# Optimization experiments

Hardware: AMD Instinct MI355X
Metric: run time of the kernel (lower is better)

Reference implementation:

```python
import jax, jax.numpy as jnp
import numpy as np

B, S, D = 2, 2048, 1024
H = 16
HD = D // H  # 64
SCALE = HD ** 0.5


def setup_inputs() -> dict:
    key = jax.random.key(0)
    ks = jax.random.split(key, 7)
    return {
        "query": jax.random.normal(ks[0], (B, S, D), dtype=jnp.float32),
        "key": jax.random.normal(ks[1], (B, S, D), dtype=jnp.float32),
        "value": jax.random.normal(ks[2], (B, S, D), dtype=jnp.float32),
        "W_qkv_w": jax.random.normal(ks[3], (3 * D, 3 * D), dtype=jnp.float32) * (1.0 / np.sqrt(3 * D)),
        "W_qkv_b": jax.random.normal(ks[4], (3 * D,), dtype=jnp.float32) * 0.02,
        "W_o_w": jax.random.normal(ks[5], (D, D), dtype=jnp.float32) * (1.0 / np.sqrt(D)),
        "W_o_b": jax.random.normal(ks[6], (D,), dtype=jnp.float32) * 0.02,
    }


def _split_heads(x):
    # [B,S,D] -> [B,H,S,HD]
    return x.reshape(B, S, H, HD).transpose(0, 2, 1, 3)


def reference(query, key, value, W_qkv_w, W_qkv_b, W_o_w, W_o_b):
    # fused QKV projection: concat then Linear(3D, 3D)  (torch: x @ W.T + b)
    qkv = jnp.concatenate([query, key, value], axis=-1)
    qkv = qkv @ W_qkv_w.T + W_qkv_b
    q, k, v = jnp.split(qkv, 3, axis=-1)
    q, k, v = _split_heads(q), _split_heads(k), _split_heads(v)
    # naive attention: materializes [B,H,S,S]
    scores = jnp.einsum('bhqd,bhkd->bhqk', q, k) / SCALE
    probs = jax.nn.softmax(scores, axis=-1)
    attn = jnp.einsum('bhqk,bhkd->bhqd', probs, v)
    # combine heads: [B,H,S,HD] -> [B,S,D]
    attn = attn.transpose(0, 2, 1, 3).reshape(B, S, D)
    return attn @ W_o_w.T + W_o_b
```

## Files before the change

### kernel.cpp

```cpp
#include <hip/hip_runtime.h>
#include <cmath>

#define BS   2
#define SEQ  2048
#define DM   1024
#define NH   16
#define HD   64
#define D3   3072
#define MROWS 4096
#define KVBLK 64
#define QBLK  128
#define NTILES (SEQ / KVBLK)

typedef _Float16 f16;
typedef __attribute__((ext_vector_type(4))) _Float16 half4;
typedef __attribute__((ext_vector_type(8))) _Float16 half8;
typedef __attribute__((ext_vector_type(4))) float f32x4;
typedef unsigned int u32;
typedef __attribute__((ext_vector_type(4))) u32 u32x4;

__device__ __forceinline__ void async_cp16(const void* g, void* s) {
    __builtin_amdgcn_global_load_lds(
        (const __attribute__((address_space(1))) u32*)g,
        (__attribute__((address_space(3))) u32*)s, 16, 0, 0);
}

__global__ __launch_bounds__(256) void conv_concat_kernel(
    const float* __restrict__ q, const float* __restrict__ k,
    const float* __restrict__ v, f16* __restrict__ out)
{
    const int seg = blockIdx.x;
    const int row = blockIdx.y;
    const int c   = threadIdx.x * 4;
    const float* src = (seg == 0 ? q : (seg == 1 ? k : v)) + (size_t)row * DM + c;
    float4 x = *(const float4*)src;
    half4 h = {(f16)x.x, (f16)x.y, (f16)x.z, (f16)x.w};
    *(half4*)&out[(size_t)row * D3 + seg * DM + c] = h;
}

__global__ __launch_bounds__(256) void conv_plain_kernel(
    const float* __restrict__ src, f16* __restrict__ dst, int n4)
{
    int i = blockIdx.x * 256 + threadIdx.x;
    const int stride = gridDim.x * 256;
    for (; i < n4; i += stride) {
        float4 x = *(const float4*)&src[(size_t)i * 4];
        half4 h = {(f16)x.x, (f16)x.y, (f16)x.z, (f16)x.w};
        *(half4*)&dst[(size_t)i * 4] = h;
    }
}

template<int KDIM, int NDIM, bool F16OUT>
__global__ __launch_bounds__(256) void gemm_f16_kernel(
    const f16* __restrict__ A, const f16* __restrict__ W,
    const float* __restrict__ bias, void* __restrict__ Cout)
{
    __shared__ f16 As[128 * 32];
    __shared__ f16 Ws[128 * 32];

    const int tid  = threadIdx.x;
    const int lane = tid & 63;
    const int wave = tid >> 6;
    const int l15  = lane & 15;
    const int lg   = lane >> 4;
    const int wm   = wave >> 1;
    const int wn   = wave & 1;

    const int cpx = gridDim.x >> 3;
    const int lid = (blockIdx.x & 7) * cpx + (blockIdx.x >> 3);
    const int NT  = NDIM / 128;
    const int tM0 = (lid / NT) * 128;
    const int tN0 = (lid % NT) * 128;

    const int srow = lane >> 2;
    const int sch  = lane & 3;
    const int ssc  = sch ^ ((srow >> 1) & 3);

    const f16* gA0 = A + (size_t)(tM0 + wave * 32      + srow) * KDIM + ssc * 8;
    const f16* gA1 = A + (size_t)(tM0 + wave * 32 + 16 + srow) * KDIM + ssc * 8;
    const f16* gW0 = W + (size_t)(tN0 + wave * 32      + srow) * KDIM + ssc * 8;
    const f16* gW1 = W + (size_t)(tN0 + wave * 32 + 16 + srow) * KDIM + ssc * 8;
    f16* lA0 = &As[(wave * 32)      * 32];
    f16* lA1 = &As[(wave * 32 + 16) * 32];
    f16* lW0 = &Ws[(wave * 32)      * 32];
    f16* lW1 = &Ws[(wave * 32 + 16) * 32];

    f32x4 acc[4][4];
#pragma unroll
    for (int i = 0; i < 4; ++i)
#pragma unroll
        for (int j = 0; j < 4; ++j) acc[i][j] = (f32x4){0.f, 0.f, 0.f, 0.f};

    const int fsw = (lg ^ ((l15 >> 1) & 3)) * 8;
    int aoff[4], woff[4];
#pragma unroll
    for (int mi = 0; mi < 4; ++mi) aoff[mi] = (wm * 64 + mi * 16 + l15) * 32 + fsw;
#pragma unroll
    for (int ni = 0; ni < 4; ++ni) woff[ni] = (wn * 64 + ni * 16 + l15) * 32 + fsw;

    for (int k0 = 0; k0 < KDIM; k0 += 32) {
        __syncthreads();
        async_cp16(gA0 + k0, lA0);
        async_cp16(gA1 + k0, lA1);
        async_cp16(gW0 + k0, lW0);
        async_cp16(gW1 + k0, lW1);
        __syncthreads();

        half8 af[4], wf[4];
#pragma unroll
        for (int mi = 0; mi < 4; ++mi) af[mi] = *(half8*)&As[aoff[mi]];
#pragma unroll
        for (int ni = 0; ni < 4; ++ni) wf[ni] = *(half8*)&Ws[woff[ni]];
#pragma unroll
        for (int mi = 0; mi < 4; ++mi)
#pragma unroll
            for (int ni = 0; ni < 4; ++ni)
                acc[mi][ni] = __builtin_amdgcn_mfma_f32_16x16x32_f16(
                    af[mi], wf[ni], acc[mi][ni], 0, 0, 0);
    }

    float bv[4];
#pragma unroll
    for (int ni = 0; ni < 4; ++ni) bv[ni] = bias[tN0 + wn * 64 + ni * 16 + l15];

#pragma unroll
    for (int mi = 0; mi < 4; ++mi)
#pragma unroll
        for (int ni = 0; ni < 4; ++ni)
#pragma unroll
            for (int r = 0; r < 4; ++r) {
                const int m   = tM0 + wm * 64 + mi * 16 + lg * 4 + r;
                const int col = tN0 + wn * 64 + ni * 16 + l15;
                const float val = acc[mi][ni][r] + bv[ni];
                if constexpr (F16OUT)
                    ((f16*)Cout)[(size_t)m * NDIM + col] = (f16)val;
                else
                    ((float*)Cout)[(size_t)m * NDIM + col] = val;
            }
}


#define V_STORE(VtN, va, vb) do {                                             \
    u32x4 aw_ = __builtin_bit_cast(u32x4, va);                                \
    u32x4 bw_ = __builtin_bit_cast(u32x4, vb);                                \
    _Pragma("unroll")                                                         \
    for (int wd_ = 0; wd_ < 4; ++wd_) {                                       \
        u32 lo_ = __builtin_amdgcn_perm(bw_[wd_], aw_[wd_], 0x05040100u);     \
        u32 hi_ = __builtin_amdgcn_perm(bw_[wd_], aw_[wd_], 0x07060302u);     \
        const int dl_ = vd0 + 2 * wd_;                                        \
        const int dh_ = dl_ + 1;                                              \
        *(u32*)&VtN[dl_ * KVBLK + (((vp >> 2) ^ (dl_ & 7) ^ (dl_ >> 3)) * 8)  \
                    + 2 * (vp & 3)] = lo_;                                    \
        *(u32*)&VtN[dh_ * KVBLK + (((vp >> 2) ^ (dh_ & 7) ^ (dh_ >> 3)) * 8)  \
                    + 2 * (vp & 3)] = hi_;                                    \
    }                                                                         \
} while (0)

#define ATTN_STEP(KhC, VtC, KhN, VtN, TT, PF) do {                            \
    half8 va_ = {}, vb_ = {};                                                 \
    if (PF) {                                                                 \
        const size_t nro_ = (size_t)((TT) + 1) * KVBLK;                       \
        async_cp16(kxsrc + (nro_ + wave * 16 +     krow_l) * D3,              \
                   &KhN[(wave * 16) * HD]);                                   \
        async_cp16(kxsrc + (nro_ + wave * 16 + 8 + krow_l) * D3,              \
                   &KhN[(wave * 16 + 8) * HD]);                               \
        va_ = *(const half8*)(vsrc0 + nro_ * D3);                             \
        vb_ = *(const half8*)(vsrc0 + nro_ * D3 + D3);                        \
    }                                                                         \
    f32x4 sc[2][4];                                                           \
    _Pragma("unroll")                                                         \
    for (int rt = 0; rt < 2; ++rt)                                            \
        _Pragma("unroll")                                                     \
        for (int ct = 0; ct < 4; ++ct) sc[rt][ct] = (f32x4){0.f,0.f,0.f,0.f}; \
    __builtin_amdgcn_s_setprio(1);                                            \
    _Pragma("unroll")                                                         \
    for (int ct = 0; ct < 4; ++ct) {                                          \
        const int krow = ct * 16 + l15;                                       \
        _Pragma("unroll")                                                     \
        for (int ks = 0; ks < 2; ++ks) {                                      \
            half8 kf = *(half8*)&KhC[krow * HD +                              \
                                     (((ks * 4 + lg) ^ (krow & 7)) * 8)];     \
            _Pragma("unroll")                                                 \
            for (int rt = 0; rt < 2; ++rt)                                    \
                sc[rt][ct] = __builtin_amdgcn_mfma_f32_16x16x32_f16(          \
                    qf[rt][ks], kf, sc[rt][ct], 0, 0, 0);                     \
        }                                                                     \
    }                                                                         \
    __builtin_amdgcn_s_setprio(0);                                            \
    _Pragma("unroll")                                                         \
    for (int rt = 0; rt < 2; ++rt)                                            \
        _Pragma("unroll")                                                     \
        for (int ct = 0; ct < 4; ++ct)                                        \
            _Pragma("unroll")                                                 \
            for (int r = 0; r < 4; ++r) sc[rt][ct][r] *= 0.125f;              \
    _Pragma("unroll")                                                         \
    for (int rt = 0; rt < 2; ++rt) {                                          \
        float mt[4];                                                          \
        _Pragma("unroll")                                                     \
        for (int r = 0; r < 4; ++r)                                           \
            mt[r] = fmaxf(fmaxf(sc[rt][0][r], sc[rt][1][r]),                  \
                          fmaxf(sc[rt][2][r], sc[rt][3][r]));                 \
        _Pragma("unroll")                                                     \
        for (int m = 1; m < 16; m <<= 1)                                      \
            _Pragma("unroll")                                                 \
            for (int r = 0; r < 4; ++r)                                       \
                mt[r] = fmaxf(mt[r], __shfl_xor(mt[r], m));                   \
        float alpha[4], mn[4];                                                \
        _Pragma("unroll")                                                     \
        for (int r = 0; r < 4; ++r) {                                         \
            mn[r] = fmaxf(mrun[rt][r], mt[r]);                                \
            alpha[r] = __expf(mrun[rt][r] - mn[r]);                           \
            mrun[rt][r] = mn[r];                                              \
        }                                                                     \
        float ls[4] = {0.f, 0.f, 0.f, 0.f};                                   \
        _Pragma("unroll")                                                     \
        for (int ct = 0; ct < 4; ++ct) {                                      \
            f32x4 v = sc[rt][ct];                                             \
            _Pragma("unroll")                                                 \
            for (int r = 0; r < 4; ++r) {                                     \
                v[r] = __expf(v[r] - mn[r]);                                  \
                ls[r] += v[r];                                                \
                const int qq = rt * 16 + lg * 4 + r;                          \
                const int chP = (ct * 2 + (l15 >> 3)) ^ (lg << 1);            \
                Pl[pbase + qq * KVBLK + chP * 8 + (l15 & 7)] = (f16)v[r];     \
            }                                                                 \
        }                                                                     \
        _Pragma("unroll")                                                     \
        for (int m = 1; m < 16; m <<= 1)                                      \
            _Pragma("unroll")                                                 \
            for (int r = 0; r < 4; ++r) ls[r] += __shfl_xor(ls[r], m);        \
        _Pragma("unroll")                                                     \
        for (int r = 0; r < 4; ++r)                                           \
            lrun[rt][r] = lrun[rt][r] * alpha[r] + ls[r];                     \
        _Pragma("unroll")                                                     \
        for (int dct = 0; dct < 4; ++dct)                                     \
            _Pragma("unroll")                                                 \
            for (int r = 0; r < 4; ++r) oacc[rt][dct][r] *= alpha[r];         \
    }                                                                         \
    __builtin_amdgcn_s_setprio(1);                                            \
    _Pragma("unroll")                                                         \
    for (int ks2 = 0; ks2 < 2; ++ks2) {                                       \
        half8 pa[2];                                                          \
        _Pragma("unroll")                                                     \
        for (int rt = 0; rt < 2; ++rt) {                                      \
            const int qq = rt * 16 + l15;                                     \
            const int chR = (ks2 * 4 + lg) ^ ((l15 >> 2) << 1);               \
            pa[rt] = *(half8*)&Pl[pbase + qq * KVBLK + chR * 8];              \
        }                                                                     \
        _Pragma("unroll")                                                     \
        for (int dct = 0; dct < 4; ++dct) {                                   \
            const int d = dct * 16 + l15;                                     \
            half8 vf = *(half8*)&VtC[d * KVBLK +                              \
                        (((ks2 * 4 + lg) ^ (d & 7) ^ (d >> 3)) * 8)];         \
            _Pragma("unroll")                                                 \
            for (int rt = 0; rt < 2; ++rt)                                    \
                oacc[rt][dct] = __builtin_amdgcn_mfma_f32_16x16x32_f16(       \
                    pa[rt], vf, oacc[rt][dct], 0, 0, 0);                      \
        }                                                                     \
    }                                                                         \
    __builtin_amdgcn_s_setprio(0);                                            \
    if (PF) { V_STORE(VtN, va_, vb_); }                                       \
    __syncthreads();                                                          \
} while (0)

__global__ __launch_bounds__(256, 2) void attn_mfma_kernel(
    const f16* __restrict__ qkvh, f16* __restrict__ attnh)
{
    __shared__ f16 Kh0[KVBLK * HD];
    __shared__ f16 Kh1[KVBLK * HD];
    __shared__ f16 Vt0[HD * KVBLK];
    __shared__ f16 Vt1[HD * KVBLK];
    __shared__ f16 Pl[4 * 32 * KVBLK];

    const int tid  = threadIdx.x;
    const int lane = tid & 63;
    const int wave = tid >> 6;
    const int l15  = lane & 15;
    const int lg   = lane >> 4;

    const int nq  = SEQ / QBLK;
    const int bid = blockIdx.x;
    const int b   = bid / (NH * nq);
    const int h   = (bid / nq) % NH;
    const int qc  = bid % nq;
    const int q0  = qc * QBLK + wave * 32;
    const size_t bS = (size_t)b * SEQ;

    const int krow_l = lane >> 3;
    const int kschk  = (lane & 7) ^ krow_l;
    const f16* kxsrc = qkvh + bS * D3 + DM + h * HD + kschk * 8;

    const int vp  = tid >> 3;
    const int vd0 = (tid & 7) * 8;
    const f16* vsrc0 = qkvh + (bS + 2 * vp) * D3 + 2 * DM + h * HD + vd0;

    half8 qf[2][2];
#pragma unroll
    for (int rt = 0; rt < 2; ++rt)
#pragma unroll
        for (int ks = 0; ks < 2; ++ks)
            qf[rt][ks] = *(const half8*)&qkvh[(bS + q0 + rt * 16 + l15) * D3 +
                                              h * HD + ks * 32 + lg * 8];

    f32x4 oacc[2][4];
#pragma unroll
    for (int rt = 0; rt < 2; ++rt)
#pragma unroll
        for (int dct = 0; dct < 4; ++dct) oacc[rt][dct] = (f32x4){0.f, 0.f, 0.f, 0.f};

    float mrun[2][4], lrun[2][4];
#pragma unroll
    for (int rt = 0; rt < 2; ++rt)
#pragma unroll
        for (int r = 0; r < 4; ++r) { mrun[rt][r] = -INFINITY; lrun[rt][r] = 0.f; }

    const int pbase = wave * 32 * KVBLK;

    {
        async_cp16(kxsrc + (size_t)(wave * 16 +     krow_l) * D3, &Kh0[(wave * 16) * HD]);
        async_cp16(kxsrc + (size_t)(wave * 16 + 8 + krow_l) * D3, &Kh0[(wave * 16 + 8) * HD]);
        half8 va_ = *(const half8*)(vsrc0);
        half8 vb_ = *(const half8*)(vsrc0 + D3);
        V_STORE(Vt0, va_, vb_);
        __syncthreads();
    }

    for (int t = 0; t < NTILES; t += 2) {
        ATTN_STEP(Kh0, Vt0, Kh1, Vt1, t, true);
        ATTN_STEP(Kh1, Vt1, Kh0, Vt0, t + 1, (t + 1) < (NTILES - 1));
    }

#pragma unroll
    for (int rt = 0; rt < 2; ++rt) {
        float inv[4];
#pragma unroll
        for (int r = 0; r < 4; ++r) inv[r] = 1.f / lrun[rt][r];
#pragma unroll
        for (int dct = 0; dct < 4; ++dct)
#pragma unroll
            for (int r = 0; r < 4; ++r) {
                const int qq = q0 + rt * 16 + lg * 4 + r;
                attnh[(bS + qq) * DM + h * HD + dct * 16 + l15] =
                    (f16)(oacc[rt][dct][r] * inv[r]);
            }
    }
}

extern "C" void kernel_launch(void* const* d_in, const int* in_sizes, int n_in,
                              void* d_out, int out_size, void* d_ws, size_t ws_size,
                              hipStream_t stream) {
    const float* q    = (const float*)d_in[0];
    const float* k    = (const float*)d_in[1];
    const float* v    = (const float*)d_in[2];
    const float* Wqkv = (const float*)d_in[3];
    const float* bqkv = (const float*)d_in[4];
    const float* Wo   = (const float*)d_in[5];
    const float* bo   = (const float*)d_in[6];
    float* out = (float*)d_out;

    char* ws = (char*)d_ws;
    f16* Ain    = (f16*)ws;
    f16* attn_h = (f16*)ws;
    f16* Wo_h   = (f16*)(ws + 16777216);
    f16* Wqkv_h = (f16*)(ws + 25165824);
    f16* qkv_h  = (f16*)(ws + 44040192);

    conv_concat_kernel<<<dim3(3, MROWS), 256, 0, stream>>>(q, k, v, Ain);
    conv_plain_kernel<<<2048, 256, 0, stream>>>(Wqkv, Wqkv_h, D3 * D3 / 4);

    gemm_f16_kernel<D3, D3, true><<<dim3((MROWS / 128) * (D3 / 128)), 256, 0, stream>>>(
        Ain, Wqkv_h, bqkv, qkv_h);

    attn_mfma_kernel<<<dim3(BS * NH * (SEQ / QBLK)), 256, 0, stream>>>(qkv_h, attn_h);

    conv_plain_kernel<<<512, 256, 0, stream>>>(Wo, Wo_h, DM * DM / 4);

    gemm_f16_kernel<DM, DM, false><<<dim3((MROWS / 128) * (DM / 128)), 256, 0, stream>>>(
        attn_h, Wo_h, bo, out);
}
```

Measured before the change: 242.9 us.

## Shrink attention query block to 64 rows with one 16-row tile per wave

Halves the query block so each wave handles a single 16-row tile instead of two. This cuts accumulator registers and P-tile shared memory, and raises launch bounds to 4 blocks per CU to improve occupancy and latency hiding. It also remaps block IDs across 8 groups (XCD-aware swizzle) so that blocks sharing K/V land together. In exchange, each K/V tile loaded into LDS is reused by half as many query rows, doubling K/V traffic and the per-tile load and sync overhead relative to the MFMA work.

```diff
diff --git a/kernel.cpp b/kernel.cpp
--- a/kernel.cpp
+++ b/kernel.cpp
@@ -9,7 +9,7 @@
 #define D3   3072
 #define MROWS 4096
 #define KVBLK 64
-#define QBLK  128
+#define QBLK  64
 #define NTILES (SEQ / KVBLK)
 
 typedef _Float16 f16;
@@ -167,11 +167,9 @@
         va_ = *(const half8*)(vsrc0 + nro_ * D3);                             \
         vb_ = *(const half8*)(vsrc0 + nro_ * D3 + D3);                        \
     }                                                                         \
-    f32x4 sc[2][4];                                                           \
-    _Pragma("unroll")                                                         \
-    for (int rt = 0; rt < 2; ++rt)                                            \
-        _Pragma("unroll")                                                     \
-        for (int ct = 0; ct < 4; ++ct) sc[rt][ct] = (f32x4){0.f,0.f,0.f,0.f}; \
+    f32x4 sc[4];                                                              \
+    _Pragma("unroll")                                                         \
+    for (int ct = 0; ct < 4; ++ct) sc[ct] = (f32x4){0.f, 0.f, 0.f, 0.f};      \
     __builtin_amdgcn_s_setprio(1);                                            \
     _Pragma("unroll")                                                         \
     for (int ct = 0; ct < 4; ++ct) {                                          \
@@ -180,26 +178,21 @@
         for (int ks = 0; ks < 2; ++ks) {                                      \
             half8 kf = *(half8*)&KhC[krow * HD +                              \
                                      (((ks * 4 + lg) ^ (krow & 7)) * 8)];     \
-            _Pragma("unroll")                                                 \
-            for (int rt = 0; rt < 2; ++rt)                                    \
-                sc[rt][ct] = __builtin_amdgcn_mfma_f32_16x16x32_f16(          \
-                    qf[rt][ks], kf, sc[rt][ct], 0, 0, 0);                     \
+            sc[ct] = __builtin_amdgcn_mfma_f32_16x16x32_f16(                  \
+                qf[ks], kf, sc[ct], 0, 0, 0);                                 \
         }                                                                     \
     }                                                                         \
     __builtin_amdgcn_s_setprio(0);                                            \
     _Pragma("unroll")                                                         \
-    for (int rt = 0; rt < 2; ++rt)                                            \
-        _Pragma("unroll")                                                     \
-        for (int ct = 0; ct < 4; ++ct)                                        \
-            _Pragma("unroll")                                                 \
-            for (int r = 0; r < 4; ++r) sc[rt][ct][r] *= 0.125f;              \
-    _Pragma("unroll")                                                         \
-    for (int rt = 0; rt < 2; ++rt) {                                          \
+    for (int ct = 0; ct < 4; ++ct)                                            \
+        _Pragma("unroll")                                                     \
+        for (int r = 0; r < 4; ++r) sc[ct][r] *= 0.125f;                      \
+    {                                                                         \
         float mt[4];                                                          \
         _Pragma("unroll")                                                     \
         for (int r = 0; r < 4; ++r)                                           \
-            mt[r] = fmaxf(fmaxf(sc[rt][0][r], sc[rt][1][r]),                  \
-                          fmaxf(sc[rt][2][r], sc[rt][3][r]));                 \
+            mt[r] = fmaxf(fmaxf(sc[0][r], sc[1][r]),                          \
+                          fmaxf(sc[2][r], sc[3][r]));                         \
         _Pragma("unroll")                                                     \
         for (int m = 1; m < 16; m <<= 1)                                      \
             _Pragma("unroll")                                                 \
@@ -208,19 +201,19 @@
         float alpha[4], mn[4];                                                \
         _Pragma("unroll")                                                     \
         for (int r = 0; r < 4; ++r) {                                         \
-            mn[r] = fmaxf(mrun[rt][r], mt[r]);                                \
-            alpha[r] = __expf(mrun[rt][r] - mn[r]);                           \
-            mrun[rt][r] = mn[r];                                              \
+            mn[r] = fmaxf(mrun[r], mt[r]);                                    \
+            alpha[r] = __expf(mrun[r] - mn[r]);                               \
+            mrun[r] = mn[r];                                                  \
         }                                                                     \
         float ls[4] = {0.f, 0.f, 0.f, 0.f};                                   \
         _Pragma("unroll")                                                     \
         for (int ct = 0; ct < 4; ++ct) {                                      \
-            f32x4 v = sc[rt][ct];                                             \
+            f32x4 v = sc[ct];                                                 \
             _Pragma("unroll")                                                 \
             for (int r = 0; r < 4; ++r) {                                     \
                 v[r] = __expf(v[r] - mn[r]);                                  \
                 ls[r] += v[r];                                                \
-                const int qq = rt * 16 + lg * 4 + r;                          \
+                const int qq = lg * 4 + r;                                    \
                 const int chP = (ct * 2 + (l15 >> 3)) ^ (lg << 1);            \
                 Pl[pbase + qq * KVBLK + chP * 8 + (l15 & 7)] = (f16)v[r];     \
             }                                                                 \
@@ -230,32 +223,25 @@
             _Pragma("unroll")                                                 \
             for (int r = 0; r < 4; ++r) ls[r] += __shfl_xor(ls[r], m);        \
         _Pragma("unroll")                                                     \
-        for (int r = 0; r < 4; ++r)                                           \
-            lrun[rt][r] = lrun[rt][r] * alpha[r] + ls[r];                     \
+        for (int r = 0; r < 4; ++r) lrun[r] = lrun[r] * alpha[r] + ls[r];     \
         _Pragma("unroll")                                                     \
         for (int dct = 0; dct < 4; ++dct)                                     \
             _Pragma("unroll")                                                 \
-            for (int r = 0; r < 4; ++r) oacc[rt][dct][r] *= alpha[r];         \
+            for (int r = 0; r < 4; ++r) oacc[dct][r] *= alpha[r];             \
     }                                                                         \
     __builtin_amdgcn_s_setprio(1);                                            \
     _Pragma("unroll")                                                         \
     for (int ks2 = 0; ks2 < 2; ++ks2) {                                       \
-        half8 pa[2];                                                          \
-        _Pragma("unroll")                                                     \
-        for (int rt = 0; rt < 2; ++rt) {                                      \
-            const int qq = rt * 16 + l15;                                     \
-            const int chR = (ks2 * 4 + lg) ^ ((l15 >> 2) << 1);               \
-            pa[rt] = *(half8*)&Pl[pbase + qq * KVBLK + chR * 8];              \
-        }                                                                     \
+        const int qq = l15;                                                   \
+        const int chR = (ks2 * 4 + lg) ^ ((l15 >> 2) << 1);                   \
+        half8 pa = *(half8*)&Pl[pbase + qq * KVBLK + chR * 8];                \
         _Pragma("unroll")                                                     \
         for (int dct = 0; dct < 4; ++dct) {                                   \
             const int d = dct * 16 + l15;                                     \
             half8 vf = *(half8*)&VtC[d * KVBLK +                              \
                         (((ks2 * 4 + lg) ^ (d & 7) ^ (d >> 3)) * 8)];         \
-            _Pragma("unroll")                                                 \
-            for (int rt = 0; rt < 2; ++rt)                                    \
-                oacc[rt][dct] = __builtin_amdgcn_mfma_f32_16x16x32_f16(       \
-                    pa[rt], vf, oacc[rt][dct], 0, 0, 0);                      \
+            oacc[dct] = __builtin_amdgcn_mfma_f32_16x16x32_f16(               \
+                pa, vf, oacc[dct], 0, 0, 0);                                  \
         }                                                                     \
     }                                                                         \
     __builtin_amdgcn_s_setprio(0);                                            \
@@ -263,14 +249,14 @@
     __syncthreads();                                                          \
 } while (0)
 
-__global__ __launch_bounds__(256, 2) void attn_mfma_kernel(
+__global__ __launch_bounds__(256, 4) void attn_mfma_kernel(
     const f16* __restrict__ qkvh, f16* __restrict__ attnh)
 {
     __shared__ f16 Kh0[KVBLK * HD];
     __shared__ f16 Kh1[KVBLK * HD];
     __shared__ f16 Vt0[HD * KVBLK];
     __shared__ f16 Vt1[HD * KVBLK];
-    __shared__ f16 Pl[4 * 32 * KVBLK];
+    __shared__ f16 Pl[4 * 16 * KVBLK];
 
     const int tid  = threadIdx.x;
     const int lane = tid & 63;
@@ -279,11 +265,12 @@
     const int lg   = lane >> 4;
 
     const int nq  = SEQ / QBLK;
-    const int bid = blockIdx.x;
-    const int b   = bid / (NH * nq);
-    const int h   = (bid / nq) % NH;
-    const int qc  = bid % nq;
-    const int q0  = qc * QBLK + wave * 32;
+    const int cpx = gridDim.x >> 3;
+    const int lid = (blockIdx.x & 7) * cpx + (blockIdx.x >> 3);
+    const int b   = lid / (NH * nq);
+    const int h   = (lid / nq) % NH;
+    const int qc  = lid % nq;
+    const int q0  = qc * QBLK + wave * 16;
     const size_t bS = (size_t)b * SEQ;
 
     const int krow_l = lane >> 3;
@@ -294,27 +281,21 @@
     const int vd0 = (tid & 7) * 8;
     const f16* vsrc0 = qkvh + (bS + 2 * vp) * D3 + 2 * DM + h * HD + vd0;
 
-    half8 qf[2][2];
-#pragma unroll
-    for (int rt = 0; rt < 2; ++rt)
-#pragma unroll
-        for (int ks = 0; ks < 2; ++ks)
-            qf[rt][ks] = *(const half8*)&qkvh[(bS + q0 + rt * 16 + l15) * D3 +
-                                              h * HD + ks * 32 + lg * 8];
-
-    f32x4 oacc[2][4];
-#pragma unroll
-    for (int rt = 0; rt < 2; ++rt)
-#pragma unroll
-        for (int dct = 0; dct < 4; ++dct) oacc[rt][dct] = (f32x4){0.f, 0.f, 0.f, 0.f};
-
-    float mrun[2][4], lrun[2][4];
-#pragma unroll
-    for (int rt = 0; rt < 2; ++rt)
-#pragma unroll
-        for (int r = 0; r < 4; ++r) { mrun[rt][r] = -INFINITY; lrun[rt][r] = 0.f; }
-
-    const int pbase = wave * 32 * KVBLK;
+    half8 qf[2];
+#pragma unroll
+    for (int ks = 0; ks < 2; ++ks)
+        qf[ks] = *(const half8*)&qkvh[(bS + q0 + l15) * D3 +
+                                      h * HD + ks * 32 + lg * 8];
+
+    f32x4 oacc[4];
+#pragma unroll
+    for (int dct = 0; dct < 4; ++dct) oacc[dct] = (f32x4){0.f, 0.f, 0.f, 0.f};
+
+    float mrun[4], lrun[4];
+#pragma unroll
+    for (int r = 0; r < 4; ++r) { mrun[r] = -INFINITY; lrun[r] = 0.f; }
+
+    const int pbase = wave * 16 * KVBLK;
 
     {
         async_cp16(kxsrc + (size_t)(wave * 16 +     krow_l) * D3, &Kh0[(wave * 16) * HD]);
@@ -330,18 +311,17 @@
         ATTN_STEP(Kh1, Vt1, Kh0, Vt0, t + 1, (t + 1) < (NTILES - 1));
     }
 
-#pragma unroll
-    for (int rt = 0; rt < 2; ++rt) {
+    {
         float inv[4];
 #pragma unroll
-        for (int r = 0; r < 4; ++r) inv[r] = 1.f / lrun[rt][r];
+        for (int r = 0; r < 4; ++r) inv[r] = 1.f / lrun[r];
 #pragma unroll
         for (int dct = 0; dct < 4; ++dct)
 #pragma unroll
             for (int r = 0; r < 4; ++r) {
-                const int qq = q0 + rt * 16 + lg * 4 + r;
+                const int qq = q0 + lg * 4 + r;
                 attnh[(bS + qq) * DM + h * HD + dct * 16 + l15] =
-                    (f16)(oacc[rt][dct][r] * inv[r]);
+                    (f16)(oacc[dct][r] * inv[r]);
             }
     }
 }
```

After: 253.4 us. 1.04x slower.

## Transpose attention MFMA operands so softmax rows live per lane, use exp2

Applied to the files above, without the earlier changes.

Swaps the MFMA A/B operands for both QK^T and PV so each lane owns a single query row. Row max and sum then need only two cross-lane shuffles instead of four per register. The scale is folded into an exp2 argument via FMA. P is packed with cvt_pkrtz and written with 8-byte LDS stores under a new XOR swizzle, and the output is stored as half4 vectors. Block IDs are also remapped across 8 groups, likely to spread work over XCDs for cache locality. The risks are new LDS bank-conflict patterns and round-toward-zero conversion of P.

```diff
diff --git a/kernel.cpp b/kernel.cpp
--- a/kernel.cpp
+++ b/kernel.cpp
@@ -12,11 +12,14 @@
 #define QBLK  128
 #define NTILES (SEQ / KVBLK)
 
+#define CSC 0.18033688011112042f
+
 typedef _Float16 f16;
 typedef __attribute__((ext_vector_type(4))) _Float16 half4;
 typedef __attribute__((ext_vector_type(8))) _Float16 half8;
 typedef __attribute__((ext_vector_type(4))) float f32x4;
 typedef unsigned int u32;
+typedef __attribute__((ext_vector_type(2))) u32 u32x2;
 typedef __attribute__((ext_vector_type(4))) u32 u32x4;
 
 __device__ __forceinline__ void async_cp16(const void* g, void* s) {
@@ -183,59 +186,49 @@
             _Pragma("unroll")                                                 \
             for (int rt = 0; rt < 2; ++rt)                                    \
                 sc[rt][ct] = __builtin_amdgcn_mfma_f32_16x16x32_f16(          \
-                    qf[rt][ks], kf, sc[rt][ct], 0, 0, 0);                     \
+                    kf, qf[rt][ks], sc[rt][ct], 0, 0, 0);                     \
         }                                                                     \
     }                                                                         \
     __builtin_amdgcn_s_setprio(0);                                            \
     _Pragma("unroll")                                                         \
-    for (int rt = 0; rt < 2; ++rt)                                            \
+    for (int rt = 0; rt < 2; ++rt) {                                          \
+        float mt = sc[rt][0][0];                                              \
         _Pragma("unroll")                                                     \
         for (int ct = 0; ct < 4; ++ct)                                        \
             _Pragma("unroll")                                                 \
-            for (int r = 0; r < 4; ++r) sc[rt][ct][r] *= 0.125f;              \
-    _Pragma("unroll")                                                         \
-    for (int rt = 0; rt < 2; ++rt) {                                          \
-        float mt[4];                                                          \
-        _Pragma("unroll")                                                     \
-        for (int r = 0; r < 4; ++r)                                           \
-            mt[r] = fmaxf(fmaxf(sc[rt][0][r], sc[rt][1][r]),                  \
-                          fmaxf(sc[rt][2][r], sc[rt][3][r]));                 \
-        _Pragma("unroll")                                                     \
-        for (int m = 1; m < 16; m <<= 1)                                      \
-            _Pragma("unroll")                                                 \
             for (int r = 0; r < 4; ++r)                                       \
-                mt[r] = fmaxf(mt[r], __shfl_xor(mt[r], m));                   \
-        float alpha[4], mn[4];                                                \
-        _Pragma("unroll")                                                     \
-        for (int r = 0; r < 4; ++r) {                                         \
-            mn[r] = fmaxf(mrun[rt][r], mt[r]);                                \
-            alpha[r] = __expf(mrun[rt][r] - mn[r]);                           \
-            mrun[rt][r] = mn[r];                                              \
+                if (ct || r) mt = fmaxf(mt, sc[rt][ct][r]);                   \
+        mt = fmaxf(mt, __shfl_xor(mt, 16));                                   \
+        mt = fmaxf(mt, __shfl_xor(mt, 32));                                   \
+        const float mn = fmaxf(mrun[rt], mt * CSC);                           \
+        const float alpha = exp2f(mrun[rt] - mn);                             \
+        mrun[rt] = mn;                                                        \
+        float pv_[4][4];                                                      \
+        float ls = 0.f;                                                       \
+        _Pragma("unroll")                                                     \
+        for (int ct = 0; ct < 4; ++ct)                                        \
+            _Pragma("unroll")                                                 \
+            for (int r = 0; r < 4; ++r) {                                     \
+                pv_[ct][r] = exp2f(fmaf(sc[rt][ct][r], CSC, -mn));            \
+                ls += pv_[ct][r];                                             \
+            }                                                                 \
+        ls += __shfl_xor(ls, 16);                                             \
+        ls += __shfl_xor(ls, 32);                                             \
+        lrun[rt] = lrun[rt] * alpha + ls;                                     \
+        _Pragma("unroll")                                                     \
+        for (int dct = 0; dct < 4; ++dct)                                     \
+            _Pragma("unroll")                                                 \
+            for (int r = 0; r < 4; ++r) oacc[rt][dct][r] *= alpha;            \
+        const int prow_ = pbase + (rt * 16 + l15) * KVBLK;                    \
+        _Pragma("unroll")                                                     \
+        for (int ct = 0; ct < 4; ++ct) {                                      \
+            u32 w01 = __builtin_bit_cast(u32,                                 \
+                __builtin_amdgcn_cvt_pkrtz(pv_[ct][0], pv_[ct][1]));          \
+            u32 w23 = __builtin_bit_cast(u32,                                 \
+                __builtin_amdgcn_cvt_pkrtz(pv_[ct][2], pv_[ct][3]));          \
+            *(u32x2*)&Pl[prow_ + ((4 * ct + lg) ^ l15) * 4] =                 \
+                (u32x2){w01, w23};                                            \
         }                                                                     \
-        float ls[4] = {0.f, 0.f, 0.f, 0.f};                                   \
-        _Pragma("unroll")                                                     \
-        for (int ct = 0; ct < 4; ++ct) {                                      \
-            f32x4 v = sc[rt][ct];                                             \
-            _Pragma("unroll")                                                 \
-            for (int r = 0; r < 4; ++r) {                                     \
-                v[r] = __expf(v[r] - mn[r]);                                  \
-                ls[r] += v[r];                                                \
-                const int qq = rt * 16 + lg * 4 + r;                          \
-                const int chP = (ct * 2 + (l15 >> 3)) ^ (lg << 1);            \
-                Pl[pbase + qq * KVBLK + chP * 8 + (l15 & 7)] = (f16)v[r];     \
-            }                                                                 \
-        }                                                                     \
-        _Pragma("unroll")                                                     \
-        for (int m = 1; m < 16; m <<= 1)                                      \
-            _Pragma("unroll")                                                 \
-            for (int r = 0; r < 4; ++r) ls[r] += __shfl_xor(ls[r], m);        \
-        _Pragma("unroll")                                                     \
-        for (int r = 0; r < 4; ++r)                                           \
-            lrun[rt][r] = lrun[rt][r] * alpha[r] + ls[r];                     \
-        _Pragma("unroll")                                                     \
-        for (int dct = 0; dct < 4; ++dct)                                     \
-            _Pragma("unroll")                                                 \
-            for (int r = 0; r < 4; ++r) oacc[rt][dct][r] *= alpha[r];         \
     }                                                                         \
     __builtin_amdgcn_s_setprio(1);                                            \
     _Pragma("unroll")                                                         \
@@ -243,9 +236,10 @@
         half8 pa[2];                                                          \
         _Pragma("unroll")                                                     \
         for (int rt = 0; rt < 2; ++rt) {                                      \
-            const int qq = rt * 16 + l15;                                     \
-            const int chR = (ks2 * 4 + lg) ^ ((l15 >> 2) << 1);               \
-            pa[rt] = *(half8*)&Pl[pbase + qq * KVBLK + chR * 8];              \
+            const int prow_ = pbase + (rt * 16 + l15) * KVBLK;                \
+            half4 plA_ = *(half4*)&Pl[prow_ + ((8 * ks2 + 2 * lg)     ^ l15) * 4]; \
+            half4 plB_ = *(half4*)&Pl[prow_ + ((8 * ks2 + 2 * lg + 1) ^ l15) * 4]; \
+            pa[rt] = __builtin_shufflevector(plA_, plB_, 0,1,2,3,4,5,6,7);    \
         }                                                                     \
         _Pragma("unroll")                                                     \
         for (int dct = 0; dct < 4; ++dct) {                                   \
@@ -255,7 +249,7 @@
             _Pragma("unroll")                                                 \
             for (int rt = 0; rt < 2; ++rt)                                    \
                 oacc[rt][dct] = __builtin_amdgcn_mfma_f32_16x16x32_f16(       \
-                    pa[rt], vf, oacc[rt][dct], 0, 0, 0);                      \
+                    vf, pa[rt], oacc[rt][dct], 0, 0, 0);                      \
         }                                                                     \
     }                                                                         \
     __builtin_amdgcn_s_setprio(0);                                            \
@@ -279,10 +273,11 @@
     const int lg   = lane >> 4;
 
     const int nq  = SEQ / QBLK;
-    const int bid = blockIdx.x;
-    const int b   = bid / (NH * nq);
-    const int h   = (bid / nq) % NH;
-    const int qc  = bid % nq;
+    const int cpx = gridDim.x >> 3;
+    const int lid = (blockIdx.x & 7) * cpx + (blockIdx.x >> 3);
+    const int b   = lid / (NH * nq);
+    const int h   = (lid / nq) % NH;
+    const int qc  = lid % nq;
     const int q0  = qc * QBLK + wave * 32;
     const size_t bS = (size_t)b * SEQ;
 
@@ -308,11 +303,9 @@
 #pragma unroll
         for (int dct = 0; dct < 4; ++dct) oacc[rt][dct] = (f32x4){0.f, 0.f, 0.f, 0.f};
 
-    float mrun[2][4], lrun[2][4];
-#pragma unroll
-    for (int rt = 0; rt < 2; ++rt)
-#pragma unroll
-        for (int r = 0; r < 4; ++r) { mrun[rt][r] = -INFINITY; lrun[rt][r] = 0.f; }
+    float mrun[2], lrun[2];
+#pragma unroll
+    for (int rt = 0; rt < 2; ++rt) { mrun[rt] = -INFINITY; lrun[rt] = 0.f; }
 
     const int pbase = wave * 32 * KVBLK;
 
@@ -332,17 +325,15 @@
 
 #pragma unroll
     for (int rt = 0; rt < 2; ++rt) {
-        float inv[4];
-#pragma unroll
-        for (int r = 0; r < 4; ++r) inv[r] = 1.f / lrun[rt][r];
-#pragma unroll
-        for (int dct = 0; dct < 4; ++dct)
-#pragma unroll
-            for (int r = 0; r < 4; ++r) {
-                const int qq = q0 + rt * 16 + lg * 4 + r;
-                attnh[(bS + qq) * DM + h * HD + dct * 16 + l15] =
-                    (f16)(oacc[rt][dct][r] * inv[r]);
-            }
+        const float inv = 1.f / lrun[rt];
+        const int qq = q0 + rt * 16 + l15;
+#pragma unroll
+        for (int dct = 0; dct < 4; ++dct) {
+            half4 o;
+#pragma unroll
+            for (int r = 0; r < 4; ++r) o[r] = (f16)(oacc[rt][dct][r] * inv);
+            *(half4*)&attnh[(bS + qq) * DM + h * HD + dct * 16 + 4 * lg] = o;
+        }
     }
 }
 
```

New measurement: 215.7 us. -11.2%, faster.
